# Kernel tuning notes

Hardware: AMD Instinct MI355X
Metric: run time of the kernel (lower is better)

The kernel has to match this reference:

```python
import jax, jax.numpy as jnp
import numpy as np

D = 512   # dim_features
H = 8     # n_head
B = 64    # number of studies
N = 131072  # total rows (cells)
EPS = 1e-5  # LayerNorm eps (torch default)


def setup_inputs():
    key = jax.random.key(0)
    ks = jax.random.split(key, 8)
    embedding = jax.random.normal(ks[0], (N, D), dtype=jnp.float32)
    # guarantee every study id 0..B-1 appears (original loop assumes contiguous ids)
    base = np.arange(B, dtype=np.int64)
    extra = np.asarray(jax.random.randint(ks[1], (N - B,), 0, B)).astype(np.int64)
    study_indexes = jnp.asarray(np.sort(np.concatenate([base, extra])))
    s = 0.02
    return {
        "embedding": embedding,
        "study_indexes": study_indexes,
        "W_in": jax.random.normal(ks[2], (3 * D, D), dtype=jnp.float32) * s,
        "b_in": jnp.zeros((3 * D,), jnp.float32),
        "W_o": jax.random.normal(ks[3], (D, D), dtype=jnp.float32) * s,
        "b_o": jnp.zeros((D,), jnp.float32),
        "ln1_g": jnp.ones((D,), jnp.float32),
        "ln1_b": jnp.zeros((D,), jnp.float32),
        "W1": jax.random.normal(ks[4], (2 * D, D), dtype=jnp.float32) * s,
        "b1": jnp.zeros((2 * D,), jnp.float32),
        "W2": jax.random.normal(ks[5], (D, 2 * D), dtype=jnp.float32) * s,
        "b2": jnp.zeros((D,), jnp.float32),
        "ln2_g": jnp.ones((D,), jnp.float32),
        "ln2_b": jnp.zeros((D,), jnp.float32),
    }


def _ln(x, g, b):
    m = x.mean(-1, keepdims=True)
    v = ((x - m) ** 2).mean(-1, keepdims=True)
    return (x - m) / jnp.sqrt(v + EPS) * g + b


def _pad_meta(study_indexes):
    # int indices are constants: compute ragged->padded layout with numpy
    idx = np.asarray(study_indexes)
    b = int(idx.max()) + 1
    counts = np.bincount(idx, minlength=b)
    max_n = int(counts.max())
    order = np.argsort(idx, kind='stable')
    starts = np.concatenate([np.zeros(1, np.int64), np.cumsum(counts)[:-1]])
    gid = idx[order]
    pos = np.arange(idx.shape[0], dtype=np.int64) - starts[gid]
    pad = np.arange(max_n)[None, :] >= counts[:, None]  # [b, max_n] True = padding
    return b, max_n, jnp.asarray(order), jnp.asarray(gid), jnp.asarray(pos), jnp.asarray(pad)


def _forward(embedding, meta, W_in, b_in, W_o, b_o, ln1_g, ln1_b, W1, b1, W2, b2, ln2_g, ln2_b):
    b, max_n, order, gid, pos, pad = meta
    # ragged -> padded, one fused scatter (replaces the python loop)
    x = jnp.zeros((b, max_n, D), embedding.dtype).at[gid, pos].set(embedding[order])
    # torch encoder is seq-first: axis0 = seq (len b), axis1 = batch (max_n).
    # key_padding_mask = fixed_mask.t() -> kpm[n, t] masks key token t for batch n
    kpm = pad.T  # [max_n, b]
    e = D // H
    qkv = x @ W_in.T + b_in                                  # [b, max_n, 3D]
    q, k, v = jnp.split(qkv, 3, axis=-1)
    q = q.reshape(b, max_n, H, e)
    k = k.reshape(b, max_n, H, e)
    v = v.reshape(b, max_n, H, e)
    scores = jnp.einsum('snhe,tnhe->nhst', q, k) / float(np.sqrt(e))
    scores = jnp.where(kpm[:, None, None, :], -jnp.inf, scores)
    attn = jax.nn.softmax(scores, axis=-1)
    ao = jnp.einsum('nhst,tnhe->snhe', attn, v).reshape(b, max_n, D)
    x = _ln(x + ao @ W_o.T + b_o, ln1_g, ln1_b)
    ff = jax.nn.relu(x @ W1.T + b1) @ W2.T + b2
    x = _ln(x + ff, ln2_g, ln2_b)
    return x.mean(axis=1)  # pool='mean' over dim=1 -> [b, D]


def reference(embedding, study_indexes, W_in, b_in, W_o, b_o, ln1_g, ln1_b, W1, b1, W2, b2, ln2_g, ln2_b):
    meta = _pad_meta(study_indexes)
    return _forward(embedding, meta, W_in, b_in, W_o, b_o, ln1_g, ln1_b, W1, b1, W2, b2, ln2_g, ln2_b)
```

## Files before the change

### kernel.cpp

```cpp
#include <hip/hip_runtime.h>
#include <hip/hip_bf16.h>

#define D 512
#define H 8
#define E 64
#define NSTUDY 64
#define NROWS 131072
#define D3 1536
#define D2 1024
#define LN_EPS 1e-5f
#define COVER 2560

typedef short short8 __attribute__((ext_vector_type(8)));
typedef float f32x4 __attribute__((ext_vector_type(4)));
typedef float f32x16 __attribute__((ext_vector_type(16)));
typedef unsigned int uint4v __attribute__((ext_vector_type(4)));

__device__ inline void gld_lds16(const void* g, void* l) {
    __builtin_amdgcn_global_load_lds((const __attribute__((address_space(1))) unsigned int*)g,
                                     (__attribute__((address_space(3))) unsigned int*)l, 16, 0, 0);
}

__device__ inline unsigned pkbf(float a, float b) {
    unsigned ua = __builtin_bit_cast(unsigned short, __float2bfloat16(a));
    unsigned ub = __builtin_bit_cast(unsigned short, __float2bfloat16(b));
    return ua | (ub << 16);
}

__global__ void meta_kernel(const int* __restrict__ idx, int n, int* __restrict__ meta) {
    __shared__ int starts_s[NSTUDY + 1];
    int s = threadIdx.x;
    if (s <= NSTUDY) {
        int lo = 0, hi = n;
        while (lo < hi) { int mid = (lo + hi) >> 1; if (idx[mid] < s) lo = mid + 1; else hi = mid; }
        starts_s[s] = lo;
    }
    __syncthreads();
    if (s < NSTUDY) {
        meta[1 + s]  = starts_s[s];
        meta[65 + s] = starts_s[s + 1] - starts_s[s];
    }
    __syncthreads();
    if (s == 0) {
        int mx = 0;
        for (int i = 0; i < NSTUDY; i++) mx = max(mx, starts_s[i + 1] - starts_s[i]);
        meta[0] = mx;
    }
}

__global__ void zero_kernel(float* __restrict__ p, int n) {
    int i = blockIdx.x * blockDim.x + threadIdx.x;
    if (i < n) p[i] = 0.f;
}

__global__ void cvt_kernel(const float* __restrict__ src, __hip_bfloat16* __restrict__ dst, int n) {
    int i = (blockIdx.x * blockDim.x + threadIdx.x) * 4;
    if (i + 3 < n) {
        float4 v = *reinterpret_cast<const float4*>(src + i);
        dst[i + 0] = __float2bfloat16(v.x);
        dst[i + 1] = __float2bfloat16(v.y);
        dst[i + 2] = __float2bfloat16(v.z);
        dst[i + 3] = __float2bfloat16(v.w);
    }
}

template<int EPI, bool RELU, bool OUTF, bool OUTB>
__global__ __launch_bounds__(256)
void mgemm_kernel(const __hip_bfloat16* __restrict__ A, const __hip_bfloat16* __restrict__ Wb,
                  const float* __restrict__ bias, const float* __restrict__ emb,
                  const float* __restrict__ Rbuf, float* __restrict__ Cf,
                  __hip_bfloat16* __restrict__ Cb, const int* __restrict__ meta,
                  int Nn, int K, int chunk_base, int ch_shift) {
    if (chunk_base >= meta[0]) return;
    const int tid = threadIdx.x;
    const int m0 = blockIdx.x * 128;
    const int n0 = blockIdx.y * 128;
    const int lane = tid & 63;
    const int wave = tid >> 6;
    const int wr = wave >> 1;
    const int wc = wave & 1;

    __shared__ __align__(16) unsigned short As[128 * 32];
    __shared__ __align__(16) unsigned short Bs[128 * 32];
    __shared__ int rowoff[128];

    if (EPI == 1 && tid < 128) {
        int r = m0 + tid;
        int s = r >> ch_shift;
        int n = chunk_base + (r & ((1 << ch_shift) - 1));
        rowoff[tid] = (n < meta[65 + s]) ? (meta[1 + s] + n) * D : -1;
    }

    f32x4 zero4 = {0.f, 0.f, 0.f, 0.f};
    f32x4 acc[4][4];
#pragma unroll
    for (int mi = 0; mi < 4; mi++)
#pragma unroll
        for (int ni = 0; ni < 4; ni++) acc[mi][ni] = zero4;

    const int r = lane & 15;
    const int kg = lane >> 4;
    const int wbase = (tid & ~63) * 16;

    for (int k0 = 0; k0 < K; k0 += 32) {
#pragma unroll
        for (int i = 0; i < 2; i++) {
            int flat = i * 256 + tid;
            int row = flat >> 2, q = flat & 3;
            gld_lds16(A  + (size_t)(m0 + row) * K + k0 + q * 8, (char*)As + i * 4096 + wbase);
            gld_lds16(Wb + (size_t)(n0 + row) * K + k0 + q * 8, (char*)Bs + i * 4096 + wbase);
        }
        __syncthreads();
        short8 afr[4], bfr[4];
#pragma unroll
        for (int mi = 0; mi < 4; mi++)
            afr[mi] = *reinterpret_cast<const short8*>((const char*)As + (wr * 64 + mi * 16 + r) * 64 + kg * 16);
#pragma unroll
        for (int ni = 0; ni < 4; ni++)
            bfr[ni] = *reinterpret_cast<const short8*>((const char*)Bs + (wc * 64 + ni * 16 + r) * 64 + kg * 16);
#pragma unroll
        for (int mi = 0; mi < 4; mi++)
#pragma unroll
            for (int ni = 0; ni < 4; ni++)
                acc[mi][ni] = __builtin_amdgcn_mfma_f32_16x16x32_bf16(afr[mi], bfr[ni], acc[mi][ni], 0, 0, 0);
        __syncthreads();
    }

    float bcol[4];
#pragma unroll
    for (int ni = 0; ni < 4; ni++) bcol[ni] = bias[n0 + wc * 64 + ni * 16 + r];
#pragma unroll
    for (int mi = 0; mi < 4; mi++) {
#pragma unroll
        for (int j = 0; j < 4; j++) {
            int row = m0 + wr * 64 + mi * 16 + kg * 4 + j;
            int ro = -1;
            if (EPI == 1) ro = rowoff[row - m0];
#pragma unroll
            for (int ni = 0; ni < 4; ni++) {
                int col = n0 + wc * 64 + ni * 16 + r;
                float v = acc[mi][ni][j] + bcol[ni];
                if (EPI == 1) { if (ro >= 0) v += emb[ro + col]; }
                if (EPI == 2) v += Rbuf[(size_t)row * Nn + col];
                if (RELU) v = fmaxf(v, 0.f);
                if (OUTF) Cf[(size_t)row * Nn + col] = v;
                if (OUTB) Cb[(size_t)row * Nn + col] = __float2bfloat16(v);
            }
        }
    }
}

__global__ __launch_bounds__(256)
void mattn_kernel(const __hip_bfloat16* __restrict__ QKVf, const __hip_bfloat16* __restrict__ padb,
                  __hip_bfloat16* __restrict__ AO, const int* __restrict__ meta,
                  int chunk_base, int ch_shift) {
    const int maxn = meta[0];
    if (chunk_base >= maxn) return;
    const int CH = 1 << ch_shift;
    const int j = blockIdx.x;
    const int n = chunk_base + j;
    const int wave = threadIdx.x >> 6;
    const int lane = threadIdx.x & 63;
    const int h = blockIdx.y * 4 + wave;
    const int hi = lane >> 5;
    const int l31 = lane & 31;
    const int hoff = h * E;

    __shared__ const __hip_bfloat16* rowp[64];

    if (n >= maxn) {
        uint4v z = {0u, 0u, 0u, 0u};
        unsigned short* base = (unsigned short*)(AO + ((size_t)(lane * CH + j)) * D + hoff);
#pragma unroll
        for (int q = 0; q < 8; q++) *reinterpret_cast<uint4v*>(base + q * 8) = z;
        return;
    }

    if (threadIdx.x < 64) {
        int t = threadIdx.x;
        rowp[t] = (n < meta[65 + t]) ? (QKVf + (size_t)(meta[1 + t] + n) * D3) : padb;
    }
    __syncthreads();

    const unsigned long long vmask = __ballot(n < meta[65 + lane]);
    const __hip_bfloat16* rp0 = rowp[l31];
    const __hip_bfloat16* rp1 = rowp[32 + l31];

    short8 kf[2][4], qf[2][4];
#pragma unroll
    for (int ts = 0; ts < 2; ts++)
#pragma unroll
        for (int ks = 0; ks < 4; ks++)
            kf[ts][ks] = *reinterpret_cast<const short8*>((ts ? rp1 : rp0) + D + hoff + 16 * ks + 8 * hi);
#pragma unroll
    for (int ss = 0; ss < 2; ss++)
#pragma unroll
        for (int ks = 0; ks < 4; ks++)
            qf[ss][ks] = *reinterpret_cast<const short8*>((ss ? rp1 : rp0) + hoff + 16 * ks + 8 * hi);

    f32x16 z16;
#pragma unroll
    for (int i = 0; i < 16; i++) z16[i] = 0.f;

    f32x16 st[2][2];
#pragma unroll
    for (int ts = 0; ts < 2; ts++)
#pragma unroll
        for (int ss = 0; ss < 2; ss++) {
            f32x16 a = z16;
#pragma unroll
            for (int ks = 0; ks < 4; ks++)
                a = __builtin_amdgcn_mfma_f32_32x32x16_bf16(kf[ts][ks], qf[ss][ks], a, 0, 0, 0);
            st[ts][ss] = a;
        }

    short8 vf[2][4];
#pragma unroll
    for (int et = 0; et < 2; et++)
#pragma unroll
        for (int kk = 0; kk < 4; kk++) {
            short8 f;
#pragma unroll
            for (int jj = 0; jj < 8; jj++) {
                int t = 16 * kk + 8 * hi + jj;
                f[jj] = *reinterpret_cast<const short*>(rowp[t] + 2 * D + hoff + 32 * et + l31);
            }
            vf[et][kk] = f;
        }

    f32x16 ao[2][2];
#pragma unroll
    for (int ss = 0; ss < 2; ss++)
#pragma unroll
        for (int et = 0; et < 2; et++) ao[ss][et] = z16;

#pragma unroll
    for (int ss = 0; ss < 2; ss++) {
        float p[2][16];
        float mx = -1e30f;
#pragma unroll
        for (int t2 = 0; t2 < 2; t2++)
#pragma unroll
            for (int rg = 0; rg < 16; rg++) {
                int t = 32 * t2 + (rg & 3) + 8 * (rg >> 2) + 4 * hi;
                float v = ((vmask >> t) & 1ull) ? st[t2][ss][rg] * 0.125f : -1e30f;
                p[t2][rg] = v;
                mx = fmaxf(mx, v);
            }
        mx = fmaxf(mx, __shfl_xor(mx, 32));
        float sum = 0.f;
#pragma unroll
        for (int t2 = 0; t2 < 2; t2++)
#pragma unroll
            for (int rg = 0; rg < 16; rg++) {
                float e = __expf(p[t2][rg] - mx);
                p[t2][rg] = e;
                sum += e;
            }
        sum += __shfl_xor(sum, 32);
        float inv = 1.f / sum;

#pragma unroll
        for (int kk = 0; kk < 4; kk++) {
            const int t2 = kk >> 1, bs = 8 * (kk & 1);
            unsigned w0 = pkbf(p[t2][bs + 0] * inv, p[t2][bs + 1] * inv);
            unsigned w1 = pkbf(p[t2][bs + 2] * inv, p[t2][bs + 3] * inv);
            unsigned w2 = pkbf(p[t2][bs + 4] * inv, p[t2][bs + 5] * inv);
            unsigned w3 = pkbf(p[t2][bs + 6] * inv, p[t2][bs + 7] * inv);
            unsigned x0 = __shfl_xor(w0, 32);
            unsigned x1 = __shfl_xor(w1, 32);
            unsigned x2 = __shfl_xor(w2, 32);
            unsigned x3 = __shfl_xor(w3, 32);
            uint4v au;
            au.x = hi ? x2 : w0;
            au.y = hi ? x3 : w1;
            au.z = hi ? w2 : x0;
            au.w = hi ? w3 : x1;
            short8 paf = __builtin_bit_cast(short8, au);
            ao[ss][0] = __builtin_amdgcn_mfma_f32_32x32x16_bf16(paf, vf[0][kk], ao[ss][0], 0, 0, 0);
            ao[ss][1] = __builtin_amdgcn_mfma_f32_32x32x16_bf16(paf, vf[1][kk], ao[ss][1], 0, 0, 0);
        }
    }

#pragma unroll
    for (int ss = 0; ss < 2; ss++)
#pragma unroll
        for (int et = 0; et < 2; et++)
#pragma unroll
            for (int rg = 0; rg < 16; rg++) {
                int s = 32 * ss + (rg & 3) + 8 * (rg >> 2) + 4 * hi;
                AO[((size_t)(s * CH + j)) * D + hoff + 32 * et + l31] = __float2bfloat16(ao[ss][et][rg]);
            }
}

__device__ inline void block_reduce2(float& a, float& b, float* lds) {
#pragma unroll
    for (int off = 32; off >= 1; off >>= 1) {
        a += __shfl_down(a, off);
        b += __shfl_down(b, off);
    }
    int w = threadIdx.x >> 6;
    if ((threadIdx.x & 63) == 0) { lds[w * 2] = a; lds[w * 2 + 1] = b; }
    __syncthreads();
    a = lds[0] + lds[2] + lds[4] + lds[6];
    b = lds[1] + lds[3] + lds[5] + lds[7];
    __syncthreads();
}

__global__ __launch_bounds__(256)
void ln_kernel(float* __restrict__ X, __hip_bfloat16* __restrict__ Xb16,
               const float* __restrict__ g, const float* __restrict__ b,
               const int* __restrict__ meta, int chunk_base) {
    if (chunk_base >= meta[0]) return;
    __shared__ float red[8];
    const size_t row = blockIdx.x;
    float* xr = X + row * D;
    int tid = threadIdx.x;
    float x0 = xr[tid], x1 = xr[tid + 256];
    float sum = x0 + x1, sq = x0 * x0 + x1 * x1;
    block_reduce2(sum, sq, red);
    float m = sum * (1.f / 512.f);
    float v = fmaxf(sq * (1.f / 512.f) - m * m, 0.f);
    float r = rsqrtf(v + LN_EPS);
    float y0 = (x0 - m) * r * g[tid] + b[tid];
    float y1 = (x1 - m) * r * g[tid + 256] + b[tid + 256];
    xr[tid] = y0;
    xr[tid + 256] = y1;
    Xb16[row * D + tid] = __float2bfloat16(y0);
    Xb16[row * D + tid + 256] = __float2bfloat16(y1);
}

__global__ __launch_bounds__(256)
void ln2acc_kernel(const float* __restrict__ P2, const float* __restrict__ g, const float* __restrict__ bb,
                   float* __restrict__ outsum, const int* __restrict__ meta,
                   int chunk_base, int ch_shift) {
    const int maxn = meta[0];
    if (chunk_base >= maxn) return;
    __shared__ float red[8];
    const int s = blockIdx.y;
    const int j0 = blockIdx.x * 64;
    const int tid = threadIdx.x;
    float acc0 = 0.f, acc1 = 0.f;
    for (int jj = 0; jj < 64; jj++) {
        int n = chunk_base + j0 + jj;
        if (n >= maxn) break;
        const float* xr = P2 + ((size_t)(s << ch_shift) + j0 + jj) * D;
        float x0 = xr[tid], x1 = xr[tid + 256];
        float sum = x0 + x1, sq = x0 * x0 + x1 * x1;
        block_reduce2(sum, sq, red);
        float m = sum * (1.f / 512.f);
        float v = fmaxf(sq * (1.f / 512.f) - m * m, 0.f);
        float r = rsqrtf(v + LN_EPS);
        acc0 += (x0 - m) * r * g[tid] + bb[tid];
        acc1 += (x1 - m) * r * g[tid + 256] + bb[tid + 256];
    }
    atomicAdd(&outsum[s * D + tid], acc0);
    atomicAdd(&outsum[s * D + tid + 256], acc1);
}

__global__ void final_kernel(const float* __restrict__ outsum, float* __restrict__ out,
                             const int* __restrict__ meta) {
    int i = blockIdx.x * blockDim.x + threadIdx.x;
    if (i < NSTUDY * D) out[i] = outsum[i] / (float)meta[0];
}

extern "C" void kernel_launch(void* const* d_in, const int* in_sizes, int n_in,
                              void* d_out, int out_size, void* d_ws, size_t ws_size,
                              hipStream_t stream) {
    const float* emb   = (const float*)d_in[0];
    const int*   sidx  = (const int*)  d_in[1];
    const float* W_in  = (const float*)d_in[2];
    const float* b_in  = (const float*)d_in[3];
    const float* W_o   = (const float*)d_in[4];
    const float* b_o   = (const float*)d_in[5];
    const float* ln1_g = (const float*)d_in[6];
    const float* ln1_b = (const float*)d_in[7];
    const float* W1    = (const float*)d_in[8];
    const float* b1    = (const float*)d_in[9];
    const float* W2    = (const float*)d_in[10];
    const float* b2    = (const float*)d_in[11];
    const float* ln2_g = (const float*)d_in[12];
    const float* ln2_b = (const float*)d_in[13];

    const size_t FIXED = 4326400ull + 3072ull
                       + (size_t)NROWS * D * 2ull
                       + (size_t)NROWS * D3 * 2ull;
    int ch_shift = 9;
    while (ch_shift > 6 && FIXED + ((size_t)NSTUDY << ch_shift) * 8192ull > ws_size) ch_shift--;
    const int CH = 1 << ch_shift;
    const int MC = NSTUDY * CH;
    const int NC = COVER >> ch_shift;

    char* ws = (char*)d_ws;
    int*   meta   = (int*)ws;
    float* outsum = (float*)(ws + 1024);
    __hip_bfloat16* Wi_b = (__hip_bfloat16*)(ws + 132096);
    __hip_bfloat16* Wo_b = (__hip_bfloat16*)(ws + 1704960);
    __hip_bfloat16* W1_b = (__hip_bfloat16*)(ws + 2229248);
    __hip_bfloat16* W2_b = (__hip_bfloat16*)(ws + 3277824);
    __hip_bfloat16* padb = (__hip_bfloat16*)(ws + 4326400);
    __hip_bfloat16* embB = (__hip_bfloat16*)(ws + 4329472);
    __hip_bfloat16* QKVf = (__hip_bfloat16*)(ws + 4329472 + (size_t)NROWS * D * 2ull);
    char* cbase = ws + FIXED;
    __hip_bfloat16* AOb  = (__hip_bfloat16*)(cbase);
    float*          X1   = (float*)         (cbase + (size_t)MC * 1024);
    __hip_bfloat16* X1b  = (__hip_bfloat16*)(cbase + (size_t)MC * 3072);
    __hip_bfloat16* FF   = (__hip_bfloat16*)(cbase + (size_t)MC * 4096);
    float*          P2   = (float*)         (cbase + (size_t)MC * 6144);

    meta_kernel<<<1, 128, 0, stream>>>(sidx, NROWS, meta);
    zero_kernel<<<(NSTUDY * D + 255) / 256, 256, 0, stream>>>(outsum, NSTUDY * D);
    cvt_kernel<<<(D3 * D / 4 + 255) / 256, 256, 0, stream>>>(W_in, Wi_b, D3 * D);
    cvt_kernel<<<(D * D / 4 + 255) / 256, 256, 0, stream>>>(W_o, Wo_b, D * D);
    cvt_kernel<<<(D2 * D / 4 + 255) / 256, 256, 0, stream>>>(W1, W1_b, D2 * D);
    cvt_kernel<<<(D * D2 / 4 + 255) / 256, 256, 0, stream>>>(W2, W2_b, D * D2);
    cvt_kernel<<<(D3 / 4 + 255) / 256, 256, 0, stream>>>(b_in, padb, D3);
    cvt_kernel<<<(NROWS * D / 4 + 255) / 256, 256, 0, stream>>>(emb, embB, NROWS * D);

    mgemm_kernel<0, false, false, true><<<dim3(NROWS / 128, D3 / 128), 256, 0, stream>>>(
        embB, Wi_b, b_in, nullptr, nullptr, nullptr, QKVf, meta, D3, D, 0, ch_shift);

    for (int c = 0; c < NC; c++) {
        int cb = c * CH;
        mattn_kernel<<<dim3(CH, H / 4), 256, 0, stream>>>(QKVf, padb, AOb, meta, cb, ch_shift);
        mgemm_kernel<1, false, true, false><<<dim3(MC / 128, D / 128), 256, 0, stream>>>(
            AOb, Wo_b, b_o, emb, nullptr, X1, nullptr, meta, D, D, cb, ch_shift);
        ln_kernel<<<MC, 256, 0, stream>>>(X1, X1b, ln1_g, ln1_b, meta, cb);
        mgemm_kernel<0, true, false, true><<<dim3(MC / 128, D2 / 128), 256, 0, stream>>>(
            X1b, W1_b, b1, nullptr, nullptr, nullptr, FF, meta, D2, D, cb, ch_shift);
        mgemm_kernel<2, false, true, false><<<dim3(MC / 128, D / 128), 256, 0, stream>>>(
            FF, W2_b, b2, nullptr, X1, P2, nullptr, meta, D, D2, cb, ch_shift);
        ln2acc_kernel<<<dim3(CH / 64, NSTUDY), 256, 0, stream>>>(
            P2, ln2_g, ln2_b, outsum, meta, cb, ch_shift);
    }
    final_kernel<<<(NSTUDY * D + 255) / 256, 256, 0, stream>>>(outsum, (float*)d_out, meta);
}
```

Baseline: 2.592 ms.

## Deepen GEMM K-tile to 64 with XOR-swizzled LDS, XCD-aware block mapping, tail chunking

The GEMM now stages 64-wide K slices per iteration, issuing two MFMA sub-steps per barrier pair. An XOR swizzle on the LDS layout is meant to avoid bank conflicts on the wider rows. The grid becomes 1D and blocks are remapped so that consecutive tiles land on the same XCD, which should improve L2 reuse. The chunk schedule also covers the 2048..2560 tail with 128-row chunks rather than full-size chunks, cutting wasted padded work. The trade-offs are doubled LDS use per block, which may lower occupancy, and more kernel launches for the tail.

```diff
diff --git a/kernel.cpp b/kernel.cpp
--- a/kernel.cpp
+++ b/kernel.cpp
@@ -9,7 +9,6 @@
 #define D3 1536
 #define D2 1024
 #define LN_EPS 1e-5f
-#define COVER 2560
 
 typedef short short8 __attribute__((ext_vector_type(8)));
 typedef float f32x4 __attribute__((ext_vector_type(4)));
@@ -70,24 +69,26 @@
                   const float* __restrict__ bias, const float* __restrict__ emb,
                   const float* __restrict__ Rbuf, float* __restrict__ Cf,
                   __hip_bfloat16* __restrict__ Cb, const int* __restrict__ meta,
-                  int Nn, int K, int chunk_base, int ch_shift) {
+                  int Nn, int K, int nb, int chunk_base, int ch_shift) {
     if (chunk_base >= meta[0]) return;
     const int tid = threadIdx.x;
-    const int m0 = blockIdx.x * 128;
-    const int n0 = blockIdx.y * 128;
+    const int q = gridDim.x >> 3;
+    const int L = (blockIdx.x & 7) * q + (blockIdx.x >> 3);
+    const int n0 = (L % nb) * 128;
+    const int m0 = (L / nb) * 128;
     const int lane = tid & 63;
     const int wave = tid >> 6;
     const int wr = wave >> 1;
     const int wc = wave & 1;
 
-    __shared__ __align__(16) unsigned short As[128 * 32];
-    __shared__ __align__(16) unsigned short Bs[128 * 32];
+    __shared__ __align__(16) unsigned short As[128 * 64];
+    __shared__ __align__(16) unsigned short Bs[128 * 64];
     __shared__ int rowoff[128];
 
     if (EPI == 1 && tid < 128) {
-        int r = m0 + tid;
-        int s = r >> ch_shift;
-        int n = chunk_base + (r & ((1 << ch_shift) - 1));
+        int rr = m0 + tid;
+        int s = rr >> ch_shift;
+        int n = chunk_base + (rr & ((1 << ch_shift) - 1));
         rowoff[tid] = (n < meta[65 + s]) ? (meta[1 + s] + n) * D : -1;
     }
 
@@ -102,27 +103,33 @@
     const int kg = lane >> 4;
     const int wbase = (tid & ~63) * 16;
 
-    for (int k0 = 0; k0 < K; k0 += 32) {
-#pragma unroll
-        for (int i = 0; i < 2; i++) {
+    for (int k0 = 0; k0 < K; k0 += 64) {
+#pragma unroll
+        for (int i = 0; i < 4; i++) {
             int flat = i * 256 + tid;
-            int row = flat >> 2, q = flat & 3;
-            gld_lds16(A  + (size_t)(m0 + row) * K + k0 + q * 8, (char*)As + i * 4096 + wbase);
-            gld_lds16(Wb + (size_t)(n0 + row) * K + k0 + q * 8, (char*)Bs + i * 4096 + wbase);
+            int row = flat >> 3;
+            int p = flat & 7;
+            int ksrc = k0 + ((p ^ (row & 7)) << 3);
+            gld_lds16(A  + (size_t)(m0 + row) * K + ksrc, (char*)As + i * 4096 + wbase);
+            gld_lds16(Wb + (size_t)(n0 + row) * K + ksrc, (char*)Bs + i * 4096 + wbase);
         }
         __syncthreads();
-        short8 afr[4], bfr[4];
-#pragma unroll
-        for (int mi = 0; mi < 4; mi++)
-            afr[mi] = *reinterpret_cast<const short8*>((const char*)As + (wr * 64 + mi * 16 + r) * 64 + kg * 16);
-#pragma unroll
-        for (int ni = 0; ni < 4; ni++)
-            bfr[ni] = *reinterpret_cast<const short8*>((const char*)Bs + (wc * 64 + ni * 16 + r) * 64 + kg * 16);
-#pragma unroll
-        for (int mi = 0; mi < 4; mi++)
+#pragma unroll
+        for (int sub = 0; sub < 2; sub++) {
+            const int pp = (((sub << 2) | kg) ^ (r & 7)) * 16;
+            short8 afr[4], bfr[4];
+#pragma unroll
+            for (int mi = 0; mi < 4; mi++)
+                afr[mi] = *reinterpret_cast<const short8*>((const char*)As + (wr * 64 + mi * 16 + r) * 128 + pp);
 #pragma unroll
             for (int ni = 0; ni < 4; ni++)
-                acc[mi][ni] = __builtin_amdgcn_mfma_f32_16x16x32_bf16(afr[mi], bfr[ni], acc[mi][ni], 0, 0, 0);
+                bfr[ni] = *reinterpret_cast<const short8*>((const char*)Bs + (wc * 64 + ni * 16 + r) * 128 + pp);
+#pragma unroll
+            for (int mi = 0; mi < 4; mi++)
+#pragma unroll
+                for (int ni = 0; ni < 4; ni++)
+                    acc[mi][ni] = __builtin_amdgcn_mfma_f32_16x16x32_bf16(afr[mi], bfr[ni], acc[mi][ni], 0, 0, 0);
+        }
         __syncthreads();
     }
 
@@ -386,10 +393,9 @@
                        + (size_t)NROWS * D * 2ull
                        + (size_t)NROWS * D3 * 2ull;
     int ch_shift = 9;
-    while (ch_shift > 6 && FIXED + ((size_t)NSTUDY << ch_shift) * 8192ull > ws_size) ch_shift--;
+    while (ch_shift > 7 && FIXED + ((size_t)NSTUDY << ch_shift) * 8192ull > ws_size) ch_shift--;
     const int CH = 1 << ch_shift;
     const int MC = NSTUDY * CH;
-    const int NC = COVER >> ch_shift;
 
     char* ws = (char*)d_ws;
     int*   meta   = (int*)ws;
@@ -417,21 +423,27 @@
     cvt_kernel<<<(D3 / 4 + 255) / 256, 256, 0, stream>>>(b_in, padb, D3);
     cvt_kernel<<<(NROWS * D / 4 + 255) / 256, 256, 0, stream>>>(emb, embB, NROWS * D);
 
-    mgemm_kernel<0, false, false, true><<<dim3(NROWS / 128, D3 / 128), 256, 0, stream>>>(
-        embB, Wi_b, b_in, nullptr, nullptr, nullptr, QKVf, meta, D3, D, 0, ch_shift);
-
-    for (int c = 0; c < NC; c++) {
-        int cb = c * CH;
-        mattn_kernel<<<dim3(CH, H / 4), 256, 0, stream>>>(QKVf, padb, AOb, meta, cb, ch_shift);
-        mgemm_kernel<1, false, true, false><<<dim3(MC / 128, D / 128), 256, 0, stream>>>(
-            AOb, Wo_b, b_o, emb, nullptr, X1, nullptr, meta, D, D, cb, ch_shift);
-        ln_kernel<<<MC, 256, 0, stream>>>(X1, X1b, ln1_g, ln1_b, meta, cb);
-        mgemm_kernel<0, true, false, true><<<dim3(MC / 128, D2 / 128), 256, 0, stream>>>(
-            X1b, W1_b, b1, nullptr, nullptr, nullptr, FF, meta, D2, D, cb, ch_shift);
-        mgemm_kernel<2, false, true, false><<<dim3(MC / 128, D / 128), 256, 0, stream>>>(
-            FF, W2_b, b2, nullptr, X1, P2, nullptr, meta, D, D2, cb, ch_shift);
-        ln2acc_kernel<<<dim3(CH / 64, NSTUDY), 256, 0, stream>>>(
-            P2, ln2_g, ln2_b, outsum, meta, cb, ch_shift);
+    mgemm_kernel<0, false, false, true><<<dim3((NROWS / 128) * (D3 / 128)), 256, 0, stream>>>(
+        embB, Wi_b, b_in, nullptr, nullptr, nullptr, QKVf, meta, D3, D, D3 / 128, 0, ch_shift);
+
+    int cbs[64], shs[64], nsch = 0;
+    for (int cb = 0; cb < 2048; cb += CH) { cbs[nsch] = cb; shs[nsch++] = ch_shift; }
+    for (int cb = 2048; cb < 2560; cb += 128) { cbs[nsch] = cb; shs[nsch++] = 7; }
+
+    for (int c = 0; c < nsch; c++) {
+        const int cb = cbs[c], sh = shs[c];
+        const int CHc = 1 << sh;
+        const int MCc = NSTUDY << sh;
+        mattn_kernel<<<dim3(CHc, H / 4), 256, 0, stream>>>(QKVf, padb, AOb, meta, cb, sh);
+        mgemm_kernel<1, false, true, false><<<dim3((MCc / 128) * (D / 128)), 256, 0, stream>>>(
+            AOb, Wo_b, b_o, emb, nullptr, X1, nullptr, meta, D, D, D / 128, cb, sh);
+        ln_kernel<<<MCc, 256, 0, stream>>>(X1, X1b, ln1_g, ln1_b, meta, cb);
+        mgemm_kernel<0, true, false, true><<<dim3((MCc / 128) * (D2 / 128)), 256, 0, stream>>>(
+            X1b, W1_b, b1, nullptr, nullptr, nullptr, FF, meta, D2, D, D2 / 128, cb, sh);
+        mgemm_kernel<2, false, true, false><<<dim3((MCc / 128) * (D / 128)), 256, 0, stream>>>(
+            FF, W2_b, b2, nullptr, X1, P2, nullptr, meta, D, D2, D / 128, cb, sh);
+        ln2acc_kernel<<<dim3(CHc / 64, NSTUDY), 256, 0, stream>>>(
+            P2, ln2_g, ln2_b, outsum, meta, cb, sh);
     }
     final_kernel<<<(NSTUDY * D + 255) / 256, 256, 0, stream>>>(outsum, (float*)d_out, meta);
 }
```

Result: faster. 2.242 ms (-13.5%).
